# Performance work log

Hardware: AMD Instinct MI355X
Metric: run time of the kernel (lower is better)

## Reference

```python
import jax, jax.numpy as jnp
import numpy as np

B, T, DIN, DOUT, G = 8, 4096, 1024, 1024, 16
S = T // G  # equal-length contiguous segments


def setup_inputs() -> dict:
    key = jax.random.key(0)
    k1, k2, k3 = jax.random.split(key, 3)
    x = jax.random.normal(k1, (B, T, DIN), dtype=jnp.float32)
    # Embedding(num_groups, dim_in*dim_out) viewed as (dim_out, dim_in) per group
    W = jax.random.normal(k2, (G, DOUT, DIN), dtype=jnp.float32) * (1.0 / np.sqrt(DIN))
    b = jax.random.normal(k3, (G, DOUT), dtype=jnp.float32) * 0.02
    # sorted, contiguous, equal-length segments: [0,...,0,1,...,1,...,G-1]
    indices = jnp.repeat(jnp.arange(G, dtype=jnp.int64), S)
    return {"x": x, "W": W, "b": b, "indices": indices, "num_groups": G}


def reference(x, W, b, indices, num_groups):
    # SegmentLinear: for each contiguous segment of `indices`, apply the
    # group's linear layer out[:, sl] = x[:, sl] @ W[g].T + b[g].
    # With equal-length contiguous segments this is one grouped GEMM.
    Bc, Tc, Din = x.shape
    g = num_groups
    s = Tc // g
    xg = x.reshape(Bc, g, s, Din)                      # [B, G, S, din]
    out = jnp.einsum('bgsd,god->bgso', xg, W)          # grouped GEMM
    out = out + b[None, :, None, :]                    # per-group bias
    return out.reshape(Bc, Tc, -1)
```

## Files before the change

### kernel.cpp

```cpp
#include <hip/hip_runtime.h>

#define B_    8
#define T_    4096
#define DIN_  1024
#define DOUT_ 1024
#define G_    16
#define S_    256

#define BM 256
#define BN 256
#define BK 32
#define NT (DIN_ / BK)
#define NBUF 4

#define NX (B_ * T_ * DIN_)
#define NW (G_ * DOUT_ * DIN_)
#define WS_NEEDED ((size_t)(NX + NW) * 2)

typedef __bf16 bf16x8 __attribute__((ext_vector_type(8)));
typedef float  f32x4  __attribute__((ext_vector_type(4)));

__device__ __forceinline__ void gload_lds16(const void* g, void* l) {
    __builtin_amdgcn_global_load_lds(
        (const __attribute__((address_space(1))) unsigned int*)g,
        (__attribute__((address_space(3))) unsigned int*)l,
        16 , 0, 0);
}

__global__ __launch_bounds__(256)
void cvt_f32_bf16(const float* __restrict__ in, __bf16* __restrict__ out, int n8) {
    int i = blockIdx.x * 256 + threadIdx.x;
    const int stride = gridDim.x * 256;
    for (; i < n8; i += stride) {
        const f32x4 a = *(const f32x4*)(in + (long)i * 8);
        const f32x4 b = *(const f32x4*)(in + (long)i * 8 + 4);
        bf16x8 h;
        #pragma unroll
        for (int u = 0; u < 4; ++u) { h[u] = (__bf16)a[u]; h[u + 4] = (__bf16)b[u]; }
        *(bf16x8*)(out + (long)i * 8) = h;
    }
}

__global__ __launch_bounds__(512, 2)
void seg_gemm_bf16(const __bf16* __restrict__ Xb, const __bf16* __restrict__ Wb,
                   const float* __restrict__ Bias, float* __restrict__ Out)
{
    __shared__ __attribute__((aligned(16))) __bf16 As[NBUF][BM * BK];
    __shared__ __attribute__((aligned(16))) __bf16 Bs[NBUF][BN * BK];

    const int raw = blockIdx.x;
    const int bid = ((raw & 7) << 6) | (raw >> 3);
    const int g   = bid >> 5;
    const int mT  = (bid >> 2) & 7;
    const int nT  = bid & 3;

    const int tid  = threadIdx.x;
    const int lane = tid & 63;
    const int wid  = tid >> 6;
    const int wm   = wid >> 2;
    const int wn   = wid & 3;

    const long rowBase = (long)mT * T_ + (long)g * S_;

    const int sRow    = wid * 16 + (lane >> 2);
    const int srcSlot = (lane & 3) ^ ((lane >> 3) & 3);
    const __bf16* aSrc = Xb + (rowBase + sRow) * DIN_ + srcSlot * 8;
    const __bf16* bSrc = Wb + ((long)g * DOUT_ + (long)nT * BN + sRow) * DIN_ + srcSlot * 8;

    const int ml = lane & 15;
    const int h  = lane >> 4;
    const int sp = (h ^ ((ml >> 1) & 3)) * 8;

    f32x4 acc[8][4] = {};

#define STAGE(TT) do {                                                    \
    const int    b_ = (TT) & (NBUF - 1);                                  \
    const __bf16* a_ = aSrc + (TT) * BK;                                  \
    const __bf16* w_ = bSrc + (TT) * BK;                                  \
    gload_lds16(a_,              &As[b_][wid * 512]);                     \
    gload_lds16(a_ + 128 * DIN_, &As[b_][wid * 512 + 4096]);              \
    gload_lds16(w_,              &Bs[b_][wid * 512]);                     \
    gload_lds16(w_ + 128 * DIN_, &Bs[b_][wid * 512 + 4096]);              \
} while (0)

#define COMPUTE(TT) do {                                                  \
    const __bf16* Ab_ = &As[(TT) & (NBUF - 1)][0];                        \
    const __bf16* Bb_ = &Bs[(TT) & (NBUF - 1)][0];                        \
    bf16x8 aF[8], bF[4];                                                  \
    _Pragma("unroll")                                                     \
    for (int i_ = 0; i_ < 8; ++i_)                                        \
        aF[i_] = *(const bf16x8*)&Ab_[(wm * 128 + i_ * 16 + ml) * BK + sp]; \
    _Pragma("unroll")                                                     \
    for (int j_ = 0; j_ < 4; ++j_)                                        \
        bF[j_] = *(const bf16x8*)&Bb_[(wn * 64 + j_ * 16 + ml) * BK + sp];  \
    __builtin_amdgcn_s_setprio(1);                                        \
    _Pragma("unroll")                                                     \
    for (int i_ = 0; i_ < 8; ++i_)                                        \
        _Pragma("unroll")                                                 \
        for (int j_ = 0; j_ < 4; ++j_)                                    \
            acc[i_][j_] = __builtin_amdgcn_mfma_f32_16x16x32_bf16(        \
                aF[i_], bF[j_], acc[i_][j_], 0, 0, 0);                    \
    __builtin_amdgcn_s_setprio(0);                                        \
} while (0)

    STAGE(0); STAGE(1); STAGE(2);
    asm volatile("s_waitcnt vmcnt(8)" ::: "memory");
    __builtin_amdgcn_s_barrier();
    asm volatile("" ::: "memory");

    for (int t = 0; t < NT; ++t) {
        if (t + 3 < NT) STAGE(t + 3);
        COMPUTE(t);
        if (t + 1 < NT) {
            if (t + 3 < NT)      asm volatile("s_waitcnt vmcnt(8)" ::: "memory");
            else if (t + 2 < NT) asm volatile("s_waitcnt vmcnt(4)" ::: "memory");
            else                 asm volatile("s_waitcnt vmcnt(0)" ::: "memory");
            __builtin_amdgcn_s_barrier();
            asm volatile("" ::: "memory");
        }
    }

    const int ncolBase = nT * BN + wn * 64;
    #pragma unroll
    for (int j = 0; j < 4; ++j) {
        const int n = ncolBase + j * 16 + ml;
        const float bj = Bias[g * DOUT_ + n];
        #pragma unroll
        for (int i = 0; i < 8; ++i) {
            const long row0 = rowBase + wm * 128 + i * 16 + h * 4;
            #pragma unroll
            for (int r = 0; r < 4; ++r)
                Out[(row0 + r) * DOUT_ + n] = acc[i][j][r] + bj;
        }
    }
#undef STAGE
#undef COMPUTE
}

#define FBM 128
#define FBN 128
#define LDKF 40
__global__ __launch_bounds__(256, 2)
void seg_linear_fused(const float* __restrict__ X, const float* __restrict__ W,
                      const float* __restrict__ Bias, float* __restrict__ Out)
{
    __shared__ __attribute__((aligned(16))) __bf16 Asf[FBM * LDKF];
    __shared__ __attribute__((aligned(16))) __bf16 Bsf[FBN * LDKF];

    const int bid = blockIdx.x;
    const int g   = bid >> 7;
    const int rb  = bid & 127;
    const int mT  = rb >> 3;
    const int nT  = rb & 7;

    const int tid  = threadIdx.x;
    const int lane = tid & 63;
    const int wid  = tid >> 6;
    const int wr   = wid >> 1;
    const int wc   = wid & 1;

    const long rowBase = (long)(mT >> 1) * T_ + (long)g * S_ + (mT & 1) * FBM;

    const float* Abase = X + rowBase * DIN_;
    const float* Bbase = W + ((long)g * DOUT_ + (long)nT * FBN) * DIN_;

    const int srow = tid >> 1;
    const int scol = (tid & 1) * 16;
    const float* pA = Abase + (long)srow * DIN_ + scol;
    const float* pB = Bbase + (long)srow * DIN_ + scol;
    __bf16* wA = &Asf[srow * LDKF + scol];
    __bf16* wB = &Bsf[srow * LDKF + scol];

    f32x4 acc[4][4] = {};
    const int q8 = (lane >> 4) * 8;
    const int ml = lane & 15;

    for (int k0 = 0; k0 < DIN_; k0 += 32) {
        f32x4 va0 = *(const f32x4*)(pA + k0);
        f32x4 va1 = *(const f32x4*)(pA + k0 + 4);
        f32x4 va2 = *(const f32x4*)(pA + k0 + 8);
        f32x4 va3 = *(const f32x4*)(pA + k0 + 12);
        f32x4 vb0 = *(const f32x4*)(pB + k0);
        f32x4 vb1 = *(const f32x4*)(pB + k0 + 4);
        f32x4 vb2 = *(const f32x4*)(pB + k0 + 8);
        f32x4 vb3 = *(const f32x4*)(pB + k0 + 12);

        bf16x8 ha0, ha1, hb0, hb1;
        #pragma unroll
        for (int u = 0; u < 4; ++u) {
            ha0[u] = (__bf16)va0[u]; ha0[u + 4] = (__bf16)va1[u];
            ha1[u] = (__bf16)va2[u]; ha1[u + 4] = (__bf16)va3[u];
            hb0[u] = (__bf16)vb0[u]; hb0[u + 4] = (__bf16)vb1[u];
            hb1[u] = (__bf16)vb2[u]; hb1[u + 4] = (__bf16)vb3[u];
        }
        *(bf16x8*)(wA) = ha0; *(bf16x8*)(wA + 8) = ha1;
        *(bf16x8*)(wB) = hb0; *(bf16x8*)(wB + 8) = hb1;

        __syncthreads();

        bf16x8 aF[4], bF[4];
        #pragma unroll
        for (int i = 0; i < 4; ++i)
            aF[i] = *(const bf16x8*)&Asf[(wr * 64 + i * 16 + ml) * LDKF + q8];
        #pragma unroll
        for (int j = 0; j < 4; ++j)
            bF[j] = *(const bf16x8*)&Bsf[(wc * 64 + j * 16 + ml) * LDKF + q8];
        #pragma unroll
        for (int i = 0; i < 4; ++i)
            #pragma unroll
            for (int j = 0; j < 4; ++j)
                acc[i][j] = __builtin_amdgcn_mfma_f32_16x16x32_bf16(aF[i], bF[j], acc[i][j], 0, 0, 0);
        __syncthreads();
    }

    const int mq = lane >> 4;
    const int ncol = nT * FBN + wc * 64;
    #pragma unroll
    for (int j = 0; j < 4; ++j) {
        const int n = ncol + j * 16 + ml;
        const float bj = Bias[g * DOUT_ + n];
        #pragma unroll
        for (int i = 0; i < 4; ++i) {
            const long row0 = rowBase + wr * 64 + i * 16 + mq * 4;
            #pragma unroll
            for (int r = 0; r < 4; ++r)
                Out[(row0 + r) * DOUT_ + n] = acc[i][j][r] + bj;
        }
    }
}

extern "C" void kernel_launch(void* const* d_in, const int* in_sizes, int n_in,
                              void* d_out, int out_size, void* d_ws, size_t ws_size,
                              hipStream_t stream) {
    const float* X    = (const float*)d_in[0];
    const float* W    = (const float*)d_in[1];
    const float* Bias = (const float*)d_in[2];
    float* Out = (float*)d_out;

    if (ws_size >= WS_NEEDED) {
        __bf16* Xb = (__bf16*)d_ws;
        __bf16* Wb = Xb + NX;
        cvt_f32_bf16<<<dim3(2048), dim3(256), 0, stream>>>(X, Xb, NX / 8);
        cvt_f32_bf16<<<dim3(2048), dim3(256), 0, stream>>>(W, Wb, NW / 8);
        const int grid = G_ * (B_ * S_ / BM) * (DOUT_ / BN);
        seg_gemm_bf16<<<dim3(grid), dim3(512), 0, stream>>>(Xb, Wb, Bias, Out);
    } else {
        const int grid = G_ * (B_ * S_ / FBM) * (DOUT_ / FBN);
        seg_linear_fused<<<dim3(grid), dim3(256), 0, stream>>>(X, W, Bias, Out);
    }
}
```

Before: 169.8 us.

## Split GEMM k-step into half-tiles with interleaved staging, drop LDS swizzle, merge converts

Reworks the bf16 GEMM main loop so each k-step runs as two half-subtiles. Global-to-LDS loads for tile t+2 are issued between them, and barriers are placed to overlap loads with MFMA. It also removes the XOR swizzle on the LDS layout, which may bring back bank conflicts, and cuts the prefetch distance from three tiles to two. The two fp32-to-bf16 conversion launches are merged into one kernel to save a launch. The extra barriers per k-step add synchronisation cost.

```diff
diff --git a/kernel.cpp b/kernel.cpp
--- a/kernel.cpp
+++ b/kernel.cpp
@@ -11,7 +11,8 @@
 #define BN 256
 #define BK 32
 #define NT (DIN_ / BK)
-#define NBUF 4
+#define NSLOT 4
+#define SLOT_E (BM * BK)
 
 #define NX (B_ * T_ * DIN_)
 #define NW (G_ * DOUT_ * DIN_)
@@ -27,17 +28,33 @@
         16 , 0, 0);
 }
 
+__device__ __forceinline__ void block_sync() {
+    asm volatile("" ::: "memory");
+    __builtin_amdgcn_s_barrier();
+    asm volatile("" ::: "memory");
+}
+
+#define VMWAIT_(N) asm volatile("s_waitcnt vmcnt(" #N ")" ::: "memory")
+#define VMWAIT(N)  VMWAIT_(N)
+
 __global__ __launch_bounds__(256)
-void cvt_f32_bf16(const float* __restrict__ in, __bf16* __restrict__ out, int n8) {
+void cvt_f32_bf16_2(const float* __restrict__ inX, __bf16* __restrict__ outX, int nx8,
+                    const float* __restrict__ inW, __bf16* __restrict__ outW, int nw8) {
+    const int total = nx8 + nw8;
     int i = blockIdx.x * 256 + threadIdx.x;
     const int stride = gridDim.x * 256;
-    for (; i < n8; i += stride) {
-        const f32x4 a = *(const f32x4*)(in + (long)i * 8);
-        const f32x4 b = *(const f32x4*)(in + (long)i * 8 + 4);
+    for (; i < total; i += stride) {
+        const float* in;
+        __bf16* out;
+        long k;
+        if (i < nx8) { in = inX; out = outX; k = (long)i * 8; }
+        else         { in = inW; out = outW; k = (long)(i - nx8) * 8; }
+        const f32x4 a = *(const f32x4*)(in + k);
+        const f32x4 b = *(const f32x4*)(in + k + 4);
         bf16x8 h;
         #pragma unroll
         for (int u = 0; u < 4; ++u) { h[u] = (__bf16)a[u]; h[u + 4] = (__bf16)b[u]; }
-        *(bf16x8*)(out + (long)i * 8) = h;
+        *(bf16x8*)(out + k) = h;
     }
 }
 
@@ -45,8 +62,8 @@
 void seg_gemm_bf16(const __bf16* __restrict__ Xb, const __bf16* __restrict__ Wb,
                    const float* __restrict__ Bias, float* __restrict__ Out)
 {
-    __shared__ __attribute__((aligned(16))) __bf16 As[NBUF][BM * BK];
-    __shared__ __attribute__((aligned(16))) __bf16 Bs[NBUF][BN * BK];
+    __shared__ __attribute__((aligned(16))) __bf16 As[NSLOT * SLOT_E];
+    __shared__ __attribute__((aligned(16))) __bf16 Bs[NSLOT * SLOT_E];
 
     const int raw = blockIdx.x;
     const int bid = ((raw & 7) << 6) | (raw >> 3);
@@ -62,63 +79,91 @@
 
     const long rowBase = (long)mT * T_ + (long)g * S_;
 
-    const int sRow    = wid * 16 + (lane >> 2);
-    const int srcSlot = (lane & 3) ^ ((lane >> 3) & 3);
-    const __bf16* aSrc = Xb + (rowBase + sRow) * DIN_ + srcSlot * 8;
-    const __bf16* bSrc = Wb + ((long)g * DOUT_ + (long)nT * BN + sRow) * DIN_ + srcSlot * 8;
+    const int rch = lane >> 2;
+    const int sl4 = lane & 3;
+    const __bf16* gA0 = Xb + (rowBase + wid * 32 + rch) * DIN_ + sl4 * 8;
+    const __bf16* gA1 = gA0 + 16 * DIN_;
+    const __bf16* gB0 = Wb + ((long)g * DOUT_ + (long)nT * BN + wid * 32 + rch) * DIN_ + sl4 * 8;
+    const __bf16* gB1 = gB0 + 16 * DIN_;
+    const int dA0 = wid * 1024;
+    const int dA1 = dA0 + 512;
 
     const int ml = lane & 15;
     const int h  = lane >> 4;
-    const int sp = (h ^ ((ml >> 1) & 3)) * 8;
+    const int aOff = (wm * 128 + ml) * BK + h * 8;
+    const int bOff = (wn * 64  + ml) * BK + h * 8;
 
     f32x4 acc[8][4] = {};
 
-#define STAGE(TT) do {                                                    \
-    const int    b_ = (TT) & (NBUF - 1);                                  \
-    const __bf16* a_ = aSrc + (TT) * BK;                                  \
-    const __bf16* w_ = bSrc + (TT) * BK;                                  \
-    gload_lds16(a_,              &As[b_][wid * 512]);                     \
-    gload_lds16(a_ + 128 * DIN_, &As[b_][wid * 512 + 4096]);              \
-    gload_lds16(w_,              &Bs[b_][wid * 512]);                     \
-    gload_lds16(w_ + 128 * DIN_, &Bs[b_][wid * 512 + 4096]);              \
+#define STAGE_FULL(T) do {                                              \
+    const int so_ = ((T) & 3) * SLOT_E;                                 \
+    gload_lds16(gA0 + (T) * BK, As + so_ + dA0);                        \
+    gload_lds16(gA1 + (T) * BK, As + so_ + dA1);                        \
+    gload_lds16(gB0 + (T) * BK, Bs + so_ + dA0);                        \
+    gload_lds16(gB1 + (T) * BK, Bs + so_ + dA1);                        \
 } while (0)
 
-#define COMPUTE(TT) do {                                                  \
-    const __bf16* Ab_ = &As[(TT) & (NBUF - 1)][0];                        \
-    const __bf16* Bb_ = &Bs[(TT) & (NBUF - 1)][0];                        \
-    bf16x8 aF[8], bF[4];                                                  \
-    _Pragma("unroll")                                                     \
-    for (int i_ = 0; i_ < 8; ++i_)                                        \
-        aF[i_] = *(const bf16x8*)&Ab_[(wm * 128 + i_ * 16 + ml) * BK + sp]; \
-    _Pragma("unroll")                                                     \
-    for (int j_ = 0; j_ < 4; ++j_)                                        \
-        bF[j_] = *(const bf16x8*)&Bb_[(wn * 64 + j_ * 16 + ml) * BK + sp];  \
-    __builtin_amdgcn_s_setprio(1);                                        \
-    _Pragma("unroll")                                                     \
-    for (int i_ = 0; i_ < 8; ++i_)                                        \
-        _Pragma("unroll")                                                 \
-        for (int j_ = 0; j_ < 4; ++j_)                                    \
-            acc[i_][j_] = __builtin_amdgcn_mfma_f32_16x16x32_bf16(        \
-                aF[i_], bF[j_], acc[i_][j_], 0, 0, 0);                    \
-    __builtin_amdgcn_s_setprio(0);                                        \
+#define SUBTILE(T, DOSTAGE, DOSYNC, VMLIT) do {                         \
+    const __bf16* Ab_ = As + ((T) & 3) * SLOT_E;                        \
+    const __bf16* Bb_ = Bs + ((T) & 3) * SLOT_E;                        \
+    __bf16* AsW_ = As + (((T) + 2) & 3) * SLOT_E;                       \
+    __bf16* BsW_ = Bs + (((T) + 2) & 3) * SLOT_E;                       \
+    bf16x8 aF[4], bF[4];                                                \
+                                         \
+    _Pragma("unroll")                                                   \
+    for (int i_ = 0; i_ < 4; ++i_)                                      \
+        aF[i_] = *(const bf16x8*)&Ab_[aOff + i_ * (16 * BK)];           \
+    _Pragma("unroll")                                                   \
+    for (int j_ = 0; j_ < 4; ++j_)                                      \
+        bF[j_] = *(const bf16x8*)&Bb_[bOff + j_ * (16 * BK)];           \
+    if (DOSTAGE) {                                                      \
+        gload_lds16(gA0 + ((T) + 2) * BK, AsW_ + dA0);                  \
+        gload_lds16(gB0 + ((T) + 2) * BK, BsW_ + dA0);                  \
+    }                                                                   \
+    block_sync();                                                       \
+    __builtin_amdgcn_s_setprio(1);                                      \
+    _Pragma("unroll")                                                   \
+    for (int i_ = 0; i_ < 4; ++i_)                                      \
+        _Pragma("unroll")                                               \
+        for (int j_ = 0; j_ < 4; ++j_)                                  \
+            acc[i_][j_] = __builtin_amdgcn_mfma_f32_16x16x32_bf16(      \
+                aF[i_], bF[j_], acc[i_][j_], 0, 0, 0);                  \
+    __builtin_amdgcn_s_setprio(0);                                      \
+    block_sync();                                                       \
+              \
+    _Pragma("unroll")                                                   \
+    for (int i_ = 0; i_ < 4; ++i_)                                      \
+        aF[i_] = *(const bf16x8*)&Ab_[aOff + (4 + i_) * (16 * BK)];     \
+    if (DOSTAGE) {                                                      \
+        gload_lds16(gA1 + ((T) + 2) * BK, AsW_ + dA1);                  \
+        gload_lds16(gB1 + ((T) + 2) * BK, BsW_ + dA1);                  \
+    }                                                                   \
+    if (DOSYNC) {                                                       \
+        VMWAIT(VMLIT);          \
+        __builtin_amdgcn_s_barrier();                                   \
+        asm volatile("" ::: "memory");                                  \
+    }                                                                   \
+    __builtin_amdgcn_s_setprio(1);                                      \
+    _Pragma("unroll")                                                   \
+    for (int i_ = 0; i_ < 4; ++i_)                                      \
+        _Pragma("unroll")                                               \
+        for (int j_ = 0; j_ < 4; ++j_)                                  \
+            acc[4 + i_][j_] = __builtin_amdgcn_mfma_f32_16x16x32_bf16(  \
+                aF[i_], bF[j_], acc[4 + i_][j_], 0, 0, 0);              \
+    __builtin_amdgcn_s_setprio(0);                                      \
+    if (DOSYNC) block_sync();                                           \
 } while (0)
 
-    STAGE(0); STAGE(1); STAGE(2);
-    asm volatile("s_waitcnt vmcnt(8)" ::: "memory");
+    STAGE_FULL(0);
+    STAGE_FULL(1);
+    VMWAIT(4);
     __builtin_amdgcn_s_barrier();
     asm volatile("" ::: "memory");
 
-    for (int t = 0; t < NT; ++t) {
-        if (t + 3 < NT) STAGE(t + 3);
-        COMPUTE(t);
-        if (t + 1 < NT) {
-            if (t + 3 < NT)      asm volatile("s_waitcnt vmcnt(8)" ::: "memory");
-            else if (t + 2 < NT) asm volatile("s_waitcnt vmcnt(4)" ::: "memory");
-            else                 asm volatile("s_waitcnt vmcnt(0)" ::: "memory");
-            __builtin_amdgcn_s_barrier();
-            asm volatile("" ::: "memory");
-        }
-    }
+    for (int t = 0; t < NT - 2; ++t)
+        SUBTILE(t, true, true, 4);
+    SUBTILE(NT - 2, false, true, 0);
+    SUBTILE(NT - 1, false, false, 0);
 
     const int ncolBase = nT * BN + wn * 64;
     #pragma unroll
@@ -133,8 +178,8 @@
                 Out[(row0 + r) * DOUT_ + n] = acc[i][j][r] + bj;
         }
     }
-#undef STAGE
-#undef COMPUTE
+#undef STAGE_FULL
+#undef SUBTILE
 }
 
 #define FBM 128
@@ -240,8 +285,7 @@
     if (ws_size >= WS_NEEDED) {
         __bf16* Xb = (__bf16*)d_ws;
         __bf16* Wb = Xb + NX;
-        cvt_f32_bf16<<<dim3(2048), dim3(256), 0, stream>>>(X, Xb, NX / 8);
-        cvt_f32_bf16<<<dim3(2048), dim3(256), 0, stream>>>(W, Wb, NW / 8);
+        cvt_f32_bf16_2<<<dim3(2048), dim3(256), 0, stream>>>(X, Xb, NX / 8, W, Wb, NW / 8);
         const int grid = G_ * (B_ * S_ / BM) * (DOUT_ / BN);
         seg_gemm_bf16<<<dim3(grid), dim3(512), 0, stream>>>(Xb, Wb, Bias, Out);
     } else {
```

Result: faster. 164.2 us (-3.3%).

## Restructure bf16 GEMM into BK=64 half-tile phased pipeline and merge convert launches

Applied to the files above, without the earlier changes.

The GEMM main loop moves from BK=32 with a 4-deep ring buffer to BK=64 tiles, each split into two K-halves in a double buffer. Every tile runs as four phases that each load a fragment slice, issue part of the next prefetch, and then run 16 MFMAs between barriers, interleaving loads with matrix math at finer grain. The swizzle pattern changes to match the new layout. The two fp32-to-bf16 conversion launches are merged into one kernel to save a launch, at the cost of more barriers per K step and more intricate hand-tuned wait counts.

```diff
diff --git a/kernel.cpp b/kernel.cpp
--- a/kernel.cpp
+++ b/kernel.cpp
@@ -9,9 +9,9 @@
 
 #define BM 256
 #define BN 256
-#define BK 32
-#define NT (DIN_ / BK)
-#define NBUF 4
+#define BK 64
+#define NKT (DIN_ / BK)
+#define HALF_E 8192
 
 #define NX (B_ * T_ * DIN_)
 #define NW (G_ * DOUT_ * DIN_)
@@ -28,16 +28,23 @@
 }
 
 __global__ __launch_bounds__(256)
-void cvt_f32_bf16(const float* __restrict__ in, __bf16* __restrict__ out, int n8) {
+void cvt_f32_bf16_2(const float* __restrict__ inX, __bf16* __restrict__ outX, int nx8,
+                    const float* __restrict__ inW, __bf16* __restrict__ outW, int nw8) {
+    const int total = nx8 + nw8;
     int i = blockIdx.x * 256 + threadIdx.x;
     const int stride = gridDim.x * 256;
-    for (; i < n8; i += stride) {
-        const f32x4 a = *(const f32x4*)(in + (long)i * 8);
-        const f32x4 b = *(const f32x4*)(in + (long)i * 8 + 4);
+    for (; i < total; i += stride) {
+        const float* in;
+        __bf16* out;
+        long k;
+        if (i < nx8) { in = inX; out = outX; k = (long)i * 8; }
+        else         { in = inW; out = outW; k = (long)(i - nx8) * 8; }
+        const f32x4 a = *(const f32x4*)(in + k);
+        const f32x4 b = *(const f32x4*)(in + k + 4);
         bf16x8 h;
         #pragma unroll
         for (int u = 0; u < 4; ++u) { h[u] = (__bf16)a[u]; h[u + 4] = (__bf16)b[u]; }
-        *(bf16x8*)(out + (long)i * 8) = h;
+        *(bf16x8*)(out + k) = h;
     }
 }
 
@@ -45,8 +52,8 @@
 void seg_gemm_bf16(const __bf16* __restrict__ Xb, const __bf16* __restrict__ Wb,
                    const float* __restrict__ Bias, float* __restrict__ Out)
 {
-    __shared__ __attribute__((aligned(16))) __bf16 As[NBUF][BM * BK];
-    __shared__ __attribute__((aligned(16))) __bf16 Bs[NBUF][BN * BK];
+    __shared__ __attribute__((aligned(16))) __bf16 As[4 * HALF_E];
+    __shared__ __attribute__((aligned(16))) __bf16 Bs[4 * HALF_E];
 
     const int raw = blockIdx.x;
     const int bid = ((raw & 7) << 6) | (raw >> 3);
@@ -56,69 +63,93 @@
 
     const int tid  = threadIdx.x;
     const int lane = tid & 63;
-    const int wid  = tid >> 6;
-    const int wm   = wid >> 2;
-    const int wn   = wid & 3;
+    const int w    = tid >> 6;
+    const int wm   = w >> 2;
+    const int wn   = w & 3;
 
     const long rowBase = (long)mT * T_ + (long)g * S_;
-
-    const int sRow    = wid * 16 + (lane >> 2);
-    const int srcSlot = (lane & 3) ^ ((lane >> 3) & 3);
-    const __bf16* aSrc = Xb + (rowBase + sRow) * DIN_ + srcSlot * 8;
-    const __bf16* bSrc = Wb + ((long)g * DOUT_ + (long)nT * BN + sRow) * DIN_ + srcSlot * 8;
-
-    const int ml = lane & 15;
-    const int h  = lane >> 4;
-    const int sp = (h ^ ((ml >> 1) & 3)) * 8;
+    const long colBase = (long)g * DOUT_ + (long)nT * BN;
+
+    const int srow = w * 16 + (lane >> 2);
+    const int scol = ((lane & 3) ^ ((lane >> 4) & 3)) * 8;
+    const __bf16* gA = Xb + (rowBase + srow) * DIN_ + scol;
+    const __bf16* gB = Wb + (colBase + srow) * DIN_ + scol;
+    const int dOff = w * 512 + lane * 8;
+
+    const int ml  = lane & 15;
+    const int h   = lane >> 4;
+    const int hx8 = (h ^ ((ml >> 2) & 3)) * 8;
 
     f32x4 acc[8][4] = {};
 
-#define STAGE(TT) do {                                                    \
-    const int    b_ = (TT) & (NBUF - 1);                                  \
-    const __bf16* a_ = aSrc + (TT) * BK;                                  \
-    const __bf16* w_ = bSrc + (TT) * BK;                                  \
-    gload_lds16(a_,              &As[b_][wid * 512]);                     \
-    gload_lds16(a_ + 128 * DIN_, &As[b_][wid * 512 + 4096]);              \
-    gload_lds16(w_,              &Bs[b_][wid * 512]);                     \
-    gload_lds16(w_ + 128 * DIN_, &Bs[b_][wid * 512 + 4096]);              \
-} while (0)
-
-#define COMPUTE(TT) do {                                                  \
-    const __bf16* Ab_ = &As[(TT) & (NBUF - 1)][0];                        \
-    const __bf16* Bb_ = &Bs[(TT) & (NBUF - 1)][0];                        \
-    bf16x8 aF[8], bF[4];                                                  \
-    _Pragma("unroll")                                                     \
-    for (int i_ = 0; i_ < 8; ++i_)                                        \
-        aF[i_] = *(const bf16x8*)&Ab_[(wm * 128 + i_ * 16 + ml) * BK + sp]; \
-    _Pragma("unroll")                                                     \
-    for (int j_ = 0; j_ < 4; ++j_)                                        \
-        bF[j_] = *(const bf16x8*)&Bb_[(wn * 64 + j_ * 16 + ml) * BK + sp];  \
-    __builtin_amdgcn_s_setprio(1);                                        \
-    _Pragma("unroll")                                                     \
-    for (int i_ = 0; i_ < 8; ++i_)                                        \
-        _Pragma("unroll")                                                 \
-        for (int j_ = 0; j_ < 4; ++j_)                                    \
-            acc[i_][j_] = __builtin_amdgcn_mfma_f32_16x16x32_bf16(        \
-                aF[i_], bF[j_], acc[i_][j_], 0, 0, 0);                    \
-    __builtin_amdgcn_s_setprio(0);                                        \
-} while (0)
-
-    STAGE(0); STAGE(1); STAGE(2);
-    asm volatile("s_waitcnt vmcnt(8)" ::: "memory");
+#define HA(T, KH) (As + ((((T) & 1) << 1) + (KH)) * HALF_E)
+#define HB(T, KH) (Bs + ((((T) & 1) << 1) + (KH)) * HALF_E)
+#define STG_A(T, KH) do {                                                  \
+    const __bf16* p_ = gA + (T) * BK + (KH) * 32;                          \
+    gload_lds16(p_,              HA(T, KH) + dOff);                        \
+    gload_lds16(p_ + 128 * DIN_, HA(T, KH) + dOff + 4096);                 \
+} while (0)
+#define STG_B(T, KH) do {                                                  \
+    const __bf16* p_ = gB + (T) * BK + (KH) * 32;                          \
+    gload_lds16(p_,              HB(T, KH) + dOff);                        \
+    gload_lds16(p_ + 128 * DIN_, HB(T, KH) + dOff + 4096);                 \
+} while (0)
+
+#define VMW(N)  asm volatile("s_waitcnt vmcnt(" #N ")" ::: "memory")
+#define NOPV    ((void)0)
+
+#define PH(T, KH, ILO, NEWB, STAGE, VM, ENDBAR) do {                       \
+    const __bf16* Ah_ = HA(T, KH);                                         \
+    if (NEWB) {                                                            \
+        const __bf16* Bh_ = HB(T, KH);                                     \
+        _Pragma("unroll")                                                  \
+        for (int j_ = 0; j_ < 4; ++j_)                                     \
+            bF[j_] = *(const bf16x8*)&Bh_[(wn * 64 + j_ * 16 + ml) * 32 + hx8]; \
+    }                                                                      \
+    _Pragma("unroll")                                                      \
+    for (int i_ = 0; i_ < 4; ++i_)                                         \
+        aF[i_] = *(const bf16x8*)&Ah_[(wm * 128 + ((ILO) + i_) * 16 + ml) * 32 + hx8]; \
+    STAGE;                                                                 \
+    asm volatile("" ::: "memory");                                         \
+    __builtin_amdgcn_s_barrier();                                          \
+    asm volatile("s_waitcnt lgkmcnt(0)" ::: "memory");                     \
+    __builtin_amdgcn_sched_barrier(0);                                     \
+    __builtin_amdgcn_s_setprio(1);                                         \
+    _Pragma("unroll")                                                      \
+    for (int i_ = 0; i_ < 4; ++i_)                                         \
+        _Pragma("unroll")                                                  \
+        for (int j_ = 0; j_ < 4; ++j_)                                     \
+            acc[(ILO) + i_][j_] = __builtin_amdgcn_mfma_f32_16x16x32_bf16( \
+                aF[i_], bF[j_], acc[(ILO) + i_][j_], 0, 0, 0);             \
+    __builtin_amdgcn_s_setprio(0);                                         \
+    VM;                                                                    \
+    if (ENDBAR) {                                                          \
+        asm volatile("" ::: "memory");                                     \
+        __builtin_amdgcn_s_barrier();                                      \
+        asm volatile("" ::: "memory");                                     \
+    }                                                                      \
+} while (0)
+
+#define TILE(T, DS01, DS23, VM, LAST) do {                                 \
+    bf16x8 aF[4], bF[4];                                                   \
+    PH(T, 0, 0, true,  if (DS01) STG_A((T) + 1, 1), NOPV, true);           \
+    PH(T, 0, 4, false, if (DS01) STG_B((T) + 1, 1), NOPV, true);           \
+    PH(T, 1, 0, true,  if (DS23) STG_A((T) + 2, 0), NOPV, true);           \
+    PH(T, 1, 4, false, if (DS23) STG_B((T) + 2, 0), VM, !(LAST));          \
+} while (0)
+
+    STG_A(0, 0); STG_B(0, 0); STG_A(0, 1); STG_B(0, 1);
+    STG_A(1, 0); STG_B(1, 0);
+    VMW(4);
     __builtin_amdgcn_s_barrier();
     asm volatile("" ::: "memory");
 
-    for (int t = 0; t < NT; ++t) {
-        if (t + 3 < NT) STAGE(t + 3);
-        COMPUTE(t);
-        if (t + 1 < NT) {
-            if (t + 3 < NT)      asm volatile("s_waitcnt vmcnt(8)" ::: "memory");
-            else if (t + 2 < NT) asm volatile("s_waitcnt vmcnt(4)" ::: "memory");
-            else                 asm volatile("s_waitcnt vmcnt(0)" ::: "memory");
-            __builtin_amdgcn_s_barrier();
-            asm volatile("" ::: "memory");
-        }
-    }
+    for (int T = 0; T < 14; T += 2) {
+        TILE(T,     true, true, VMW(4), false);
+        TILE(T + 1, true, true, VMW(4), false);
+    }
+    TILE(14, true,  false, VMW(0), false);
+    TILE(15, false, false, NOPV,   true);
 
     const int ncolBase = nT * BN + wn * 64;
     #pragma unroll
@@ -133,8 +164,12 @@
                 Out[(row0 + r) * DOUT_ + n] = acc[i][j][r] + bj;
         }
     }
-#undef STAGE
-#undef COMPUTE
+#undef TILE
+#undef PH
+#undef STG_A
+#undef STG_B
+#undef HA
+#undef HB
 }
 
 #define FBM 128
@@ -240,8 +275,7 @@
     if (ws_size >= WS_NEEDED) {
         __bf16* Xb = (__bf16*)d_ws;
         __bf16* Wb = Xb + NX;
-        cvt_f32_bf16<<<dim3(2048), dim3(256), 0, stream>>>(X, Xb, NX / 8);
-        cvt_f32_bf16<<<dim3(2048), dim3(256), 0, stream>>>(W, Wb, NW / 8);
+        cvt_f32_bf16_2<<<dim3(2048), dim3(256), 0, stream>>>(X, Xb, NX / 8, W, Wb, NW / 8);
         const int grid = G_ * (B_ * S_ / BM) * (DOUT_ / BN);
         seg_gemm_bf16<<<dim3(grid), dim3(512), 0, stream>>>(Xb, Wb, Bias, Out);
     } else {
```

After: 155.9 us. -8.2%, faster.
